# Performance work log

Hardware: AMD Instinct MI355X
Metric: run time of the kernel (lower is better)

## Reference

```python
import jax, jax.numpy as jnp
import numpy as np

BETA = 1.0  # config.beta
B, G, K, E2 = 1024, 512, 128, 128


def setup_inputs() -> dict:
    key = jax.random.key(0)
    k1, k2, k3, k4, k5 = jax.random.split(key, 5)
    s = 0.05
    return {
        "images": jax.random.normal(k1, (B, G), dtype=jnp.float32),
        "wimg": jax.random.normal(k2, (G, K), dtype=jnp.float32) * s,    # project.weight.T
        "wrec": jax.random.normal(k3, (K, E2), dtype=jnp.float32) * s,   # rec.weight.T
        "wrec2": jax.random.normal(k4, (K + 1, E2), dtype=jnp.float32) * s,  # rec2.weight.T
        "wimg2": jax.random.normal(k5, (G, K, K + 1), dtype=jnp.float32) * s,  # img2.weight.T.reshape(K+1,K,G).T
    }


def _soft_assign(x, codes):
    # x: [B, D], codes: [D, C] -> softmax over C of -beta * mean_D (x - codes)^2
    xh = -jnp.mean((x[:, :, None] - codes[None]) ** 2, axis=1) * BETA  # [B, C]
    return jax.nn.softmax(xh, axis=-1)


def reference(images, wimg, wrec, wrec2, wimg2):
    # ---- encode ----
    xp = _soft_assign(images, wimg)            # [B, K]
    lat = xp @ wrec                            # [B, E2]
    xp = _soft_assign(lat, wrec.T)             # [B, K] (codes are wrec.T: [E2, K])
    idx = jnp.argmax(xp, axis=-1)              # [B] hard component
    xwimg = jnp.transpose(wimg2[:, idx, :], (1, 0, 2))   # [B, G, K+1]
    base = wimg[:, idx].T[:, :, None]                     # [B, G, 1]
    xd = images[:, :, None] - base - xwimg                # [B, G, K+1]
    xh2 = -jnp.mean(xd ** 2, axis=1) * BETA               # [B, K+1]
    xp2 = jax.nn.softmax(xh2, axis=-1)
    lat2 = xp2 @ wrec2                                    # [B, E2]
    # ---- decode (ret='rec', n_step>=1) ----
    xp_d = _soft_assign(lat, wrec.T)           # [B, K]
    xp2_d = _soft_assign(lat2, wrec2.T)        # [B, K+1]
    wimgg = wimg[:, :, None] + wimg2           # [G, K, K+1]
    # tensordot(xp_d[:, :, None]*xp2_d[:, None, :], wimgg.permute(1,2,0), 2)
    xrec = jnp.einsum('bk,bj,gkj->bg', xp_d, xp2_d, wimgg)  # [B, G]
    # ---- loss ----
    loss = jnp.mean((xrec - images) ** 2, axis=-1)  # [B]
    return loss
```

## Files before the change

### kernel.cpp

```cpp
#include <hip/hip_runtime.h>

#define B_    1024
#define G_    512
#define K_    128
#define J_    129
#define JP_   132
#define E2_   128
#define KK_   16512
#define KK2_  16896
#define KKE2_ 17024
#define KKP_  17408
#define SPLITS 16
#define KCHUNK 1088
#define BK_   32
#define KSTEPS 34
#define GS_   8

using short8 = __attribute__((ext_vector_type(8))) short;
using f32x4  = __attribute__((ext_vector_type(4))) float;

__device__ __forceinline__ float bf2f(unsigned short h){
  return __uint_as_float(((unsigned int)h) << 16);
}
__device__ __forceinline__ unsigned short f2bf(float f){
  unsigned int u = __float_as_uint(f);
  u += 0x7fffu + ((u >> 16) & 1u);
  return (unsigned short)(u >> 16);
}

#define GLOAD16(gptr, ldst) __builtin_amdgcn_global_load_lds( \
    (const __attribute__((address_space(1))) unsigned int*)(gptr), \
    (__attribute__((address_space(3))) unsigned int*)(ldst), 16, 0, 0)

__device__ __forceinline__ float blockSum512(float v, float* red, int t){
  #pragma unroll
  for (int off = 32; off > 0; off >>= 1) v += __shfl_down(v, off);
  __syncthreads();
  if ((t & 63) == 0) red[t >> 6] = v;
  __syncthreads();
  float r = ((red[0] + red[1]) + (red[2] + red[3]))
          + ((red[4] + red[5]) + (red[6] + red[7]));
  __syncthreads();
  return r;
}

__device__ __forceinline__ void blockSoftmaxMS512(float x, bool act,
    float* redm, float* reds, int t, float& mo, float& so){
  float m = x, s = act ? 1.f : 0.f;
  #pragma unroll
  for (int off = 32; off > 0; off >>= 1){
    float om = __shfl_down(m, off);
    float os = __shfl_down(s, off);
    float nm = fmaxf(m, om);
    s = s*__expf(m - nm) + os*__expf(om - nm);
    m = nm;
  }
  __syncthreads();
  if ((t & 63) == 0){ redm[t >> 6] = m; reds[t >> 6] = s; }
  __syncthreads();
  float gm = redm[0], gsv = reds[0];
  #pragma unroll
  for (int w = 1; w < 8; w++){
    float om = redm[w], os = reds[w];
    float nm = fmaxf(gm, om);
    gsv = gsv*__expf(gm - nm) + os*__expf(om - nm);
    gm = nm;
  }
  mo = gm; so = gsv;
}

__device__ __forceinline__ int blockSoftmaxMSI512(float x, int idx, bool act,
    float* redm, float* reds, int* redi, int t, float& mo, float& so){
  float m = x, s = act ? 1.f : 0.f; int i = idx;
  #pragma unroll
  for (int off = 32; off > 0; off >>= 1){
    float om = __shfl_down(m, off);
    float os = __shfl_down(s, off);
    int   oi = __shfl_down(i, off);
    bool take = (om > m) || (om == m && oi < i);
    float nm = fmaxf(m, om);
    s = s*__expf(m - nm) + os*__expf(om - nm);
    i = take ? oi : i;
    m = nm;
  }
  __syncthreads();
  if ((t & 63) == 0){ redm[t >> 6] = m; reds[t >> 6] = s; redi[t >> 6] = i; }
  __syncthreads();
  float gm = redm[0], gsv = reds[0]; int gi = redi[0];
  #pragma unroll
  for (int w = 1; w < 8; w++){
    float om = redm[w], os = reds[w]; int oi = redi[w];
    bool take = (om > gm) || (om == gm && oi < gi);
    float nm = fmaxf(gm, om);
    gsv = gsv*__expf(gm - nm) + os*__expf(om - nm);
    gi = take ? oi : gi;
    gm = nm;
  }
  mo = gm; so = gsv;
  return gi;
}

__global__ __launch_bounds__(1024) void norms_kernel(
    const float* __restrict__ wimg, const float* __restrict__ wrec,
    const float* __restrict__ wrec2, float* __restrict__ c1norm,
    float* __restrict__ w3norm, float* __restrict__ w6norm,
    float* __restrict__ wrecT, float* __restrict__ wrec2T){
  int t = threadIdx.x;
  if (blockIdx.x == 0){
    __shared__ float red[8][128];
    int k = t & 127, sl = t >> 7;
    float s = 0.f;
    int g0 = sl * (G_/8);
    for (int g = g0; g < g0 + G_/8; g++){
      float v = wimg[g*K_ + k]; s += v*v;
    }
    red[sl][k] = s;
    __syncthreads();
    if (t < 128){
      float r = 0.f;
      #pragma unroll
      for (int i = 0; i < 8; i++) r += red[i][t];
      c1norm[t] = r;
    }
  } else if (blockIdx.x == 1){
    int wave = t >> 6, lane = t & 63;
    for (int k = wave; k < K_; k += 16){
      float v0 = wrec[k*E2_ + lane], v1 = wrec[k*E2_ + 64 + lane];
      float s = v0*v0 + v1*v1;
      #pragma unroll
      for (int off = 32; off > 0; off >>= 1) s += __shfl_down(s, off);
      if (lane == 0) w3norm[k] = s;
    }
  } else if (blockIdx.x == 2){
    int wave = t >> 6, lane = t & 63;
    for (int j = wave; j < J_; j += 16){
      float v0 = wrec2[j*E2_ + lane], v1 = wrec2[j*E2_ + 64 + lane];
      float s = v0*v0 + v1*v1;
      #pragma unroll
      for (int off = 32; off > 0; off >>= 1) s += __shfl_down(s, off);
      if (lane == 0) w6norm[j] = s;
    }
  } else if (blockIdx.x == 3){
    for (int n = t; n < K_*E2_; n += 1024){
      int k = n >> 7, e = n & 127;
      wrecT[e*K_ + k] = wrec[n];
    }
  } else {
    for (int n = t; n < J_*E2_; n += 1024){
      int j = n >> 7, e = n & 127;
      wrec2T[e*J_ + j] = wrec2[n];
    }
  }
}

__global__ __launch_bounds__(128) void tables_part_kernel(
    const float* __restrict__ wimg2, const float* __restrict__ wimg,
    float* __restrict__ sqp, float* __restrict__ crp,
    unsigned short* __restrict__ W2){
  int n  = blockIdx.x * 128 + threadIdx.x;
  int gs = blockIdx.y;
  int k = n / J_;
  int w2i = n + 3*k;
  float s0=0,s1=0,s2=0,s3=0, c0=0,c1=0,c2=0,c3=0;
  int gbase = gs * (G_/GS_);
  #pragma unroll 2
  for (int g = gbase; g < gbase + G_/GS_; g += 4){
    float w0 = wimg2[(size_t)(g  )*KK_ + n];
    float w1 = wimg2[(size_t)(g+1)*KK_ + n];
    float w2 = wimg2[(size_t)(g+2)*KK_ + n];
    float w3 = wimg2[(size_t)(g+3)*KK_ + n];
    W2[(size_t)(g  )*KKP_ + w2i] = f2bf(w0);
    W2[(size_t)(g+1)*KKP_ + w2i] = f2bf(w1);
    W2[(size_t)(g+2)*KKP_ + w2i] = f2bf(w2);
    W2[(size_t)(g+3)*KKP_ + w2i] = f2bf(w3);
    s0 += w0*w0; s1 += w1*w1; s2 += w2*w2; s3 += w3*w3;
    c0 += wimg[(g  )*K_ + k]*w0;
    c1 += wimg[(g+1)*K_ + k]*w1;
    c2 += wimg[(g+2)*K_ + k]*w2;
    c3 += wimg[(g+3)*K_ + k]*w3;
  }
  sqp[(size_t)gs*KK_ + n] = (s0+s1)+(s2+s3);
  crp[(size_t)gs*KK_ + n] = (c0+c1)+(c2+c3);
}
__global__ __launch_bounds__(128) void tables_reduce_kernel(
    const float* __restrict__ sqp, const float* __restrict__ crp,
    float* __restrict__ sq2, float* __restrict__ cross){
  int n = blockIdx.x * 128 + threadIdx.x;
  float s = 0.f, c = 0.f;
  #pragma unroll
  for (int gs = 0; gs < GS_; gs++){
    s += sqp[(size_t)gs*KK_ + n];
    c += crp[(size_t)gs*KK_ + n];
  }
  sq2[n] = s; cross[n] = c;
}

__global__ __launch_bounds__(128) void w2tail_kernel(
    const float* __restrict__ wimg, unsigned short* __restrict__ W2){
  int g = blockIdx.x, t = threadIdx.x;
  unsigned short* dst = W2 + (size_t)g * KKP_;
  dst[KK2_ + t]        = f2bf(wimg[g*K_ + t]);
  dst[KKE2_ + t]       = 0;
  dst[KKE2_ + 128 + t] = 0;
  dst[KKE2_ + 256 + t] = 0;
  dst[t*JP_ + 129] = 0;
  dst[t*JP_ + 130] = 0;
  dst[t*JP_ + 131] = 0;
}

__global__ __launch_bounds__(512, 8) void encdec_kernel(
    const float* __restrict__ img,  const float* __restrict__ wimg,
    const float* __restrict__ wrec, const float* __restrict__ wrec2,
    const float* __restrict__ wrecT, const float* __restrict__ wrec2T,
    const unsigned short* __restrict__ W2,
    const float* __restrict__ c1norm, const float* __restrict__ w3norm,
    const float* __restrict__ w6norm, const float* __restrict__ sq2,
    const float* __restrict__ cross, unsigned short* __restrict__ Rm){
  __shared__ __align__(16) float simg[G_];
  __shared__ float sp[K_];
  __shared__ float sqv[J_];
  __shared__ float slat[E2_];
  __shared__ float sd1[K_];
  __shared__ __align__(16) float sh16[16][128];
  __shared__ float sh4[4][K_];
  __shared__ float xtra[2];
  __shared__ float redm[8], reds[8];
  __shared__ int   redi[8];

  int t = threadIdx.x;
  int b = blockIdx.x;
  int tt = t & 127, q = t >> 7;
  int ll = t & 31, gq = t >> 5;

  simg[t] = img[b*G_ + t];
  __syncthreads();
  float a0 = simg[t];
  float imgnorm = blockSum512(a0*a0, redm, t);

  {
    float p0=0,p1=0,p2=0,p3=0;
    int g0 = gq * 32;
    #pragma unroll 4
    for (int g = g0; g < g0 + 32; g++){
      float4 wv = *(const float4*)(wimg + g*K_ + 4*ll);
      float sv = simg[g];
      p0 += sv*wv.x; p1 += sv*wv.y; p2 += sv*wv.z; p3 += sv*wv.w;
    }
    float4 st = {p0, p1, p2, p3};
    *(float4*)&sh16[gq][4*ll] = st;
  }
  __syncthreads();
  float xh1 = -3e38f, d1 = 0.f;
  if (t < 128){
    #pragma unroll
    for (int i = 0; i < 16; i++) d1 += sh16[i][t];
    sd1[t] = d1;
    xh1 = -(imgnorm - 2.f*d1 + c1norm[t]) * (1.f/512.f);
  }
  float m1, s1;
  blockSoftmaxMS512(xh1, t < 128, redm, reds, t, m1, s1);
  if (t < 128) sp[t] = __expf(xh1 - m1) / s1;
  __syncthreads();

  {
    float l0=0,l1=0;
    int k0 = q * 32;
    for (int k = k0; k < k0 + 32; k += 2){
      l0 += sp[k  ] * wrec[(k  )*E2_ + tt];
      l1 += sp[k+1] * wrec[(k+1)*E2_ + tt];
    }
    sh4[q][tt] = l0 + l1;
  }
  __syncthreads();
  float lat = (sh4[0][tt] + sh4[1][tt]) + (sh4[2][tt] + sh4[3][tt]);
  if (q == 0) slat[tt] = lat;
  float latnorm = blockSum512((q == 0) ? lat*lat : 0.f, redm, t);

  {
    float l0=0,l1=0;
    int e0 = q * 32;
    const float* rT = wrecT + tt;
    for (int e = e0; e < e0 + 32; e += 2){
      l0 += slat[e  ] * rT[(e  )*K_];
      l1 += slat[e+1] * rT[(e+1)*K_];
    }
    sh4[q][tt] = l0 + l1;
  }
  __syncthreads();
  float xh3 = -3e38f;
  if (t < 128){
    float d3 = (sh4[0][t] + sh4[1][t]) + (sh4[2][t] + sh4[3][t]);
    xh3 = -(latnorm - 2.f*d3 + w3norm[t]) * (1.f/128.f);
  }
  float m3, s3;
  int idxb = blockSoftmaxMSI512(xh3, tt, t < 128, redm, reds, redi, t, m3, s3);
  if (t < 128) sp[t] = __expf(xh3 - m3) / s3;
  float dsq = imgnorm - 2.f*sd1[idxb] + c1norm[idxb];

  {
    const unsigned short* Wb = W2 + (size_t)idxb * JP_ + 4*ll;
    float p0=0,p1=0,p2=0,p3=0;
    int g0 = gq * 32;
    #pragma unroll 4
    for (int g = g0; g < g0 + 32; g++){
      uint2 wv = *(const uint2*)(Wb + (size_t)g*KKP_);
      float sv = simg[g];
      p0 += sv * __uint_as_float(wv.x << 16);
      p1 += sv * __uint_as_float(wv.x & 0xffff0000u);
      p2 += sv * __uint_as_float(wv.y << 16);
      p3 += sv * __uint_as_float(wv.y & 0xffff0000u);
    }
    float4 st = {p0, p1, p2, p3};
    *(float4*)&sh16[gq][4*ll] = st;
  }
  if (t < 64){
    const unsigned short* Wb8 = W2 + (size_t)idxb * JP_ + 128;
    float s = 0.f;
    #pragma unroll
    for (int m = 0; m < 8; m++){
      int g = t + 64*m;
      s += simg[g] * bf2f(Wb8[(size_t)g * KKP_]);
    }
    #pragma unroll
    for (int off = 32; off > 0; off >>= 1) s += __shfl_down(s, off);
    if (t == 0) xtra[0] = s;
  }
  __syncthreads();
  float xh2 = -3e38f;
  if (t < J_){
    float di;
    if (t < 128){
      di = 0.f;
      #pragma unroll
      for (int i = 0; i < 16; i++) di += sh16[i][t];
    } else di = xtra[0];
    int nb = idxb*J_ + t;
    xh2 = -(dsq - 2.f*(di - cross[nb]) + sq2[nb]) * (1.f/512.f);
  }
  float m2, s2;
  blockSoftmaxMS512(xh2, t < J_, redm, reds, t, m2, s2);
  if (t < J_) sqv[t] = __expf(xh2 - m2) / s2;
  __syncthreads();

  {
    float lv = 0.f;
    int j0 = (q == 0) ? 0 : (q*32 + 1);
    int j1 = q*32 + 33;
    for (int j = j0; j < j1; j++)
      lv += sqv[j] * wrec2[j*E2_ + tt];
    sh4[q][tt] = lv;
  }
  __syncthreads();
  float lat2 = (sh4[0][tt] + sh4[1][tt]) + (sh4[2][tt] + sh4[3][tt]);
  if (q == 0) slat[tt] = lat2;
  float l2n = blockSum512((q == 0) ? lat2*lat2 : 0.f, redm, t);

  {
    float l0=0,l1=0;
    int e0 = q * 32;
    const float* rT = wrec2T + tt;
    for (int e = e0; e < e0 + 32; e += 2){
      l0 += slat[e  ] * rT[(e  )*J_];
      l1 += slat[e+1] * rT[(e+1)*J_];
    }
    sh4[q][tt] = l0 + l1;
  }
  if (t < 64){
    float s = slat[t]*wrec2T[t*J_ + 128] + slat[t+64]*wrec2T[(t+64)*J_ + 128];
    #pragma unroll
    for (int off = 32; off > 0; off >>= 1) s += __shfl_down(s, off);
    if (t == 0) xtra[1] = s;
  }
  __syncthreads();
  float xh6 = -3e38f;
  if (t < J_){
    float d6 = (t < 128) ? ((sh4[0][t] + sh4[1][t]) + (sh4[2][t] + sh4[3][t])) : xtra[1];
    xh6 = -(l2n - 2.f*d6 + w6norm[t]) * (1.f/128.f);
  }
  float m6, s6;
  blockSoftmaxMS512(xh6, t < J_, redm, reds, t, m6, s6);
  if (t < J_) sqv[t] = __expf(xh6 - m6) / s6;
  __syncthreads();

  unsigned int* Rrow32 = (unsigned int*)(Rm + (size_t)b * KKP_);
  int k = t / 66;
  int j2 = t - k*66;
  for (int kk2 = t; kk2 < KKP_/2; kk2 += 512){
    float v0 = 0.f, v1 = 0.f;
    if (kk2 < KK2_/2){
      int j = 2*j2;
      float pk = sp[k];
      v0 = (j   < J_) ? pk * sqv[j]   : 0.f;
      v1 = (j+1 < J_) ? pk * sqv[j+1] : 0.f;
    } else if (kk2 < KKE2_/2){
      int e = 2*(kk2 - KK2_/2);
      v0 = sp[e]; v1 = sp[e+1];
    }
    Rrow32[kk2] = (unsigned int)f2bf(v0) | ((unsigned int)f2bf(v1) << 16);
    j2 += 50;
    if (j2 >= 66){ j2 -= 66; k += 8; } else k += 7;
  }
}

__global__ __launch_bounds__(256) void gemm_kernel(
    const unsigned short* __restrict__ Rm, const unsigned short* __restrict__ W2,
    float* __restrict__ part){
  __shared__ __align__(16) unsigned int lds[8192];
  auto lds3 = (__attribute__((address_space(3))) unsigned int*)lds;
  int tid = threadIdx.x;
  int l = tid & 63;
  int wv = tid >> 6;
  int wr = (wv >> 1) * 64, wc = (wv & 1) * 64;
  int b0 = blockIdx.y * 128, g0 = blockIdx.x * 128;
  size_t kkbase = (size_t)blockIdx.z * KCHUNK;

  int srow = tid >> 2, scol = tid & 3;
  const unsigned short* ga  = Rm + (size_t)(b0 + srow)*KKP_ + kkbase + scol*8;
  const unsigned short* ga2 = ga + (size_t)64 * KKP_;
  const unsigned short* gb  = W2 + (size_t)(g0 + srow)*KKP_ + kkbase + scol*8;
  const unsigned short* gb2 = gb + (size_t)64 * KKP_;

  int lrow = l & 15, lko = (l >> 4) << 2;

  f32x4 zero4 = {0.f, 0.f, 0.f, 0.f};
  f32x4 acc[4][4];
  #pragma unroll
  for (int mi = 0; mi < 4; mi++)
    #pragma unroll
    for (int ni = 0; ni < 4; ni++) acc[mi][ni] = zero4;

  GLOAD16(ga,  lds3 + wv*256);
  GLOAD16(ga2, lds3 + 1024 + wv*256);
  GLOAD16(gb,  lds3 + 2048 + wv*256);
  GLOAD16(gb2, lds3 + 3072 + wv*256);
  ga += BK_; ga2 += BK_; gb += BK_; gb2 += BK_;

  int cur = 0;
  for (int s = 0; s < KSTEPS; s++){
    __syncthreads();
    if (s + 1 < KSTEPS){
      unsigned int nb = (cur ^ 1) * 4096;
      GLOAD16(ga,  lds3 + nb + wv*256);
      GLOAD16(ga2, lds3 + nb + 1024 + wv*256);
      GLOAD16(gb,  lds3 + nb + 2048 + wv*256);
      GLOAD16(gb2, lds3 + nb + 3072 + wv*256);
      ga += BK_; ga2 += BK_; gb += BK_; gb2 += BK_;
    }
    const unsigned int* lA = lds + cur*4096;
    const unsigned int* lB = lA + 2048;
    short8 af[4], bfv[4];
    #pragma unroll
    for (int mi = 0; mi < 4; mi++)
      af[mi] = *(const short8*)(lA + (wr + mi*16 + lrow)*16 + lko);
    #pragma unroll
    for (int ni = 0; ni < 4; ni++)
      bfv[ni] = *(const short8*)(lB + (wc + ni*16 + lrow)*16 + lko);
    #pragma unroll
    for (int mi = 0; mi < 4; mi++)
      #pragma unroll
      for (int ni = 0; ni < 4; ni++)
        acc[mi][ni] = __builtin_amdgcn_mfma_f32_16x16x32_bf16(af[mi], bfv[ni], acc[mi][ni], 0, 0, 0);
    cur ^= 1;
  }

  float* P = part + ((size_t)blockIdx.z * B_ + b0) * G_ + g0;
  int rh = (l >> 4) << 2, cl = l & 15;
  #pragma unroll
  for (int mi = 0; mi < 4; mi++)
    #pragma unroll
    for (int ni = 0; ni < 4; ni++)
      #pragma unroll
      for (int r = 0; r < 4; r++){
        int row = wr + mi*16 + rh + r;
        int col = wc + ni*16 + cl;
        P[(size_t)row*G_ + col] = acc[mi][ni][r];
      }
}

__global__ __launch_bounds__(128) void loss_kernel(
    const float* __restrict__ img, const float* __restrict__ part,
    float* __restrict__ out){
  __shared__ float redf[2];
  int t = threadIdx.x, b = blockIdx.x;
  float acc = 0.f;
  for (int g = t; g < G_; g += 128){
    float x = 0.f;
    #pragma unroll
    for (int z = 0; z < SPLITS; z++)
      x += part[((size_t)z*B_ + b)*G_ + g];
    float d = x - img[b*G_ + g];
    acc += d*d;
  }
  #pragma unroll
  for (int off = 32; off > 0; off >>= 1) acc += __shfl_down(acc, off);
  __syncthreads();
  if ((t & 63) == 0) redf[t >> 6] = acc;
  __syncthreads();
  if (t == 0) out[b] = (redf[0] + redf[1]) * (1.f/512.f);
}

extern "C" void kernel_launch(void* const* d_in, const int* in_sizes, int n_in,
                              void* d_out, int out_size, void* d_ws, size_t ws_size,
                              hipStream_t stream){
  (void)in_sizes; (void)n_in; (void)out_size; (void)ws_size;
  const float* img   = (const float*)d_in[0];
  const float* wimg  = (const float*)d_in[1];
  const float* wrec  = (const float*)d_in[2];
  const float* wrec2 = (const float*)d_in[3];
  const float* wimg2 = (const float*)d_in[4];
  float* out = (float*)d_out;

  char* ws = (char*)d_ws;
  size_t off = 0;
  auto alloc = [&](size_t bytes) -> void* {
    void* p = ws + off;
    off += (bytes + 255) & ~(size_t)255;
    return p;
  };
  unsigned short* W2   = (unsigned short*)alloc((size_t)G_ * KKP_ * 2);
  unsigned short* Rm   = (unsigned short*)alloc((size_t)B_ * KKP_ * 2);
  float* part   = (float*)alloc((size_t)SPLITS * B_ * G_ * 4);
  float* sqp    = (float*)alloc((size_t)GS_ * KK_ * 4);
  float* crp    = (float*)alloc((size_t)GS_ * KK_ * 4);
  float* sq2    = (float*)alloc((size_t)KK_ * 4);
  float* cross  = (float*)alloc((size_t)KK_ * 4);
  float* c1norm = (float*)alloc(K_ * 4);
  float* w3norm = (float*)alloc(K_ * 4);
  float* w6norm = (float*)alloc(J_ * 4);
  float* wrecT  = (float*)alloc((size_t)K_ * E2_ * 4);
  float* wrec2T = (float*)alloc((size_t)J_ * E2_ * 4);

  norms_kernel<<<dim3(5), dim3(1024), 0, stream>>>(wimg, wrec, wrec2, c1norm, w3norm, w6norm, wrecT, wrec2T);
  tables_part_kernel<<<dim3(129, GS_), dim3(128), 0, stream>>>(wimg2, wimg, sqp, crp, W2);
  tables_reduce_kernel<<<dim3(129), dim3(128), 0, stream>>>(sqp, crp, sq2, cross);
  w2tail_kernel<<<dim3(512), dim3(128), 0, stream>>>(wimg, W2);
  encdec_kernel<<<dim3(1024), dim3(512), 0, stream>>>(img, wimg, wrec, wrec2, wrecT, wrec2T, W2,
      c1norm, w3norm, w6norm, sq2, cross, Rm);
  gemm_kernel<<<dim3(4, 8, SPLITS), dim3(256), 0, stream>>>(Rm, W2, part);
  loss_kernel<<<dim3(1024), dim3(128), 0, stream>>>(img, part, out);
}
```

Measured before the change: 122.9 us.

## Process two batch rows per encdec block to share weight loads and barriers

The encode/decode kernel now handles two images per block: each weight element loaded from global memory (wimg, wrec, wrecT, wrec2, wrec2T) is reused for both rows, and the block reductions and softmaxes are paired so each barrier serves two rows. The grid halves to 512 blocks and the occupancy hint drops from 8 to 4 blocks per CU to give room for the extra registers. The cost is fewer blocks on the GPU, which leaves less parallelism to hide latency, plus doubled LDS use per block. The gather of W2 rows through idx stays per-row.

```diff
diff --git a/kernel.cpp b/kernel.cpp
--- a/kernel.cpp
+++ b/kernel.cpp
@@ -32,72 +32,96 @@
     (const __attribute__((address_space(1))) unsigned int*)(gptr), \
     (__attribute__((address_space(3))) unsigned int*)(ldst), 16, 0, 0)
 
-__device__ __forceinline__ float blockSum512(float v, float* red, int t){
-  #pragma unroll
-  for (int off = 32; off > 0; off >>= 1) v += __shfl_down(v, off);
-  __syncthreads();
-  if ((t & 63) == 0) red[t >> 6] = v;
-  __syncthreads();
-  float r = ((red[0] + red[1]) + (red[2] + red[3]))
-          + ((red[4] + red[5]) + (red[6] + red[7]));
-  __syncthreads();
-  return r;
-}
-
-__device__ __forceinline__ void blockSoftmaxMS512(float x, bool act,
-    float* redm, float* reds, int t, float& mo, float& so){
-  float m = x, s = act ? 1.f : 0.f;
+__device__ __forceinline__ void blockSum2(float v0, float v1, float* red, int t,
+                                          float& r0, float& r1){
   #pragma unroll
   for (int off = 32; off > 0; off >>= 1){
-    float om = __shfl_down(m, off);
-    float os = __shfl_down(s, off);
-    float nm = fmaxf(m, om);
-    s = s*__expf(m - nm) + os*__expf(om - nm);
-    m = nm;
-  }
-  __syncthreads();
-  if ((t & 63) == 0){ redm[t >> 6] = m; reds[t >> 6] = s; }
-  __syncthreads();
-  float gm = redm[0], gsv = reds[0];
+    v0 += __shfl_down(v0, off);
+    v1 += __shfl_down(v1, off);
+  }
+  __syncthreads();
+  if ((t & 63) == 0){ red[t >> 6] = v0; red[8 + (t >> 6)] = v1; }
+  __syncthreads();
+  r0 = ((red[0] + red[1]) + (red[2] + red[3])) + ((red[4] + red[5]) + (red[6] + red[7]));
+  r1 = ((red[8] + red[9]) + (red[10] + red[11])) + ((red[12] + red[13]) + (red[14] + red[15]));
+  __syncthreads();
+}
+
+__device__ __forceinline__ void blockSoftmaxMS2(float x0, float x1, bool act,
+    float* redm, float* reds, int t,
+    float& m0o, float& s0o, float& m1o, float& s1o){
+  float m0 = x0, s0 = act ? 1.f : 0.f;
+  float m1 = x1, s1 = act ? 1.f : 0.f;
+  #pragma unroll
+  for (int off = 32; off > 0; off >>= 1){
+    float om0 = __shfl_down(m0, off), os0 = __shfl_down(s0, off);
+    float om1 = __shfl_down(m1, off), os1 = __shfl_down(s1, off);
+    float nm0 = fmaxf(m0, om0);
+    s0 = s0*__expf(m0 - nm0) + os0*__expf(om0 - nm0); m0 = nm0;
+    float nm1 = fmaxf(m1, om1);
+    s1 = s1*__expf(m1 - nm1) + os1*__expf(om1 - nm1); m1 = nm1;
+  }
+  __syncthreads();
+  if ((t & 63) == 0){
+    redm[t >> 6] = m0; reds[t >> 6] = s0;
+    redm[8 + (t >> 6)] = m1; reds[8 + (t >> 6)] = s1;
+  }
+  __syncthreads();
+  float gm0 = redm[0], gs0 = reds[0], gm1 = redm[8], gs1 = reds[8];
   #pragma unroll
   for (int w = 1; w < 8; w++){
-    float om = redm[w], os = reds[w];
-    float nm = fmaxf(gm, om);
-    gsv = gsv*__expf(gm - nm) + os*__expf(om - nm);
-    gm = nm;
-  }
-  mo = gm; so = gsv;
-}
-
-__device__ __forceinline__ int blockSoftmaxMSI512(float x, int idx, bool act,
-    float* redm, float* reds, int* redi, int t, float& mo, float& so){
-  float m = x, s = act ? 1.f : 0.f; int i = idx;
+    float om0 = redm[w], os0 = reds[w];
+    float nm0 = fmaxf(gm0, om0);
+    gs0 = gs0*__expf(gm0 - nm0) + os0*__expf(om0 - nm0); gm0 = nm0;
+    float om1 = redm[8 + w], os1 = reds[8 + w];
+    float nm1 = fmaxf(gm1, om1);
+    gs1 = gs1*__expf(gm1 - nm1) + os1*__expf(om1 - nm1); gm1 = nm1;
+  }
+  m0o = gm0; s0o = gs0; m1o = gm1; s1o = gs1;
+}
+
+__device__ __forceinline__ void blockSoftmaxMSI2(float x0, float x1, int idx, bool act,
+    float* redm, float* reds, int* redi, int t,
+    float& m0o, float& s0o, int& i0o, float& m1o, float& s1o, int& i1o){
+  float m0 = x0, s0 = act ? 1.f : 0.f; int i0 = idx;
+  float m1 = x1, s1 = act ? 1.f : 0.f; int i1 = idx;
   #pragma unroll
   for (int off = 32; off > 0; off >>= 1){
-    float om = __shfl_down(m, off);
-    float os = __shfl_down(s, off);
-    int   oi = __shfl_down(i, off);
-    bool take = (om > m) || (om == m && oi < i);
-    float nm = fmaxf(m, om);
-    s = s*__expf(m - nm) + os*__expf(om - nm);
-    i = take ? oi : i;
-    m = nm;
-  }
-  __syncthreads();
-  if ((t & 63) == 0){ redm[t >> 6] = m; reds[t >> 6] = s; redi[t >> 6] = i; }
-  __syncthreads();
-  float gm = redm[0], gsv = reds[0]; int gi = redi[0];
+    float om0 = __shfl_down(m0, off), os0 = __shfl_down(s0, off);
+    int   oi0 = __shfl_down(i0, off);
+    float om1 = __shfl_down(m1, off), os1 = __shfl_down(s1, off);
+    int   oi1 = __shfl_down(i1, off);
+    bool tk0 = (om0 > m0) || (om0 == m0 && oi0 < i0);
+    float nm0 = fmaxf(m0, om0);
+    s0 = s0*__expf(m0 - nm0) + os0*__expf(om0 - nm0);
+    i0 = tk0 ? oi0 : i0; m0 = nm0;
+    bool tk1 = (om1 > m1) || (om1 == m1 && oi1 < i1);
+    float nm1 = fmaxf(m1, om1);
+    s1 = s1*__expf(m1 - nm1) + os1*__expf(om1 - nm1);
+    i1 = tk1 ? oi1 : i1; m1 = nm1;
+  }
+  __syncthreads();
+  if ((t & 63) == 0){
+    redm[t >> 6] = m0; reds[t >> 6] = s0; redi[t >> 6] = i0;
+    redm[8 + (t >> 6)] = m1; reds[8 + (t >> 6)] = s1; redi[8 + (t >> 6)] = i1;
+  }
+  __syncthreads();
+  float gm0 = redm[0], gs0 = reds[0]; int gi0 = redi[0];
+  float gm1 = redm[8], gs1 = reds[8]; int gi1 = redi[8];
   #pragma unroll
   for (int w = 1; w < 8; w++){
-    float om = redm[w], os = reds[w]; int oi = redi[w];
-    bool take = (om > gm) || (om == gm && oi < gi);
-    float nm = fmaxf(gm, om);
-    gsv = gsv*__expf(gm - nm) + os*__expf(om - nm);
-    gi = take ? oi : gi;
-    gm = nm;
-  }
-  mo = gm; so = gsv;
-  return gi;
+    { float om = redm[w], os = reds[w]; int oi = redi[w];
+      bool tk = (om > gm0) || (om == gm0 && oi < gi0);
+      float nm = fmaxf(gm0, om);
+      gs0 = gs0*__expf(gm0 - nm) + os*__expf(om - nm);
+      gi0 = tk ? oi : gi0; gm0 = nm; }
+    { float om = redm[8 + w], os = reds[8 + w]; int oi = redi[8 + w];
+      bool tk = (om > gm1) || (om == gm1 && oi < gi1);
+      float nm = fmaxf(gm1, om);
+      gs1 = gs1*__expf(gm1 - nm) + os*__expf(om - nm);
+      gi1 = tk ? oi : gi1; gm1 = nm; }
+  }
+  m0o = gm0; s0o = gs0; i0o = gi0; m1o = gm1; s1o = gs1; i1o = gi1;
 }
 
 __global__ __launch_bounds__(1024) void norms_kernel(
@@ -208,7 +232,7 @@
   dst[t*JP_ + 131] = 0;
 }
 
-__global__ __launch_bounds__(512, 8) void encdec_kernel(
+__global__ __launch_bounds__(512, 4) void encdec_kernel(
     const float* __restrict__ img,  const float* __restrict__ wimg,
     const float* __restrict__ wrec, const float* __restrict__ wrec2,
     const float* __restrict__ wrecT, const float* __restrict__ wrec2T,
@@ -216,187 +240,251 @@
     const float* __restrict__ c1norm, const float* __restrict__ w3norm,
     const float* __restrict__ w6norm, const float* __restrict__ sq2,
     const float* __restrict__ cross, unsigned short* __restrict__ Rm){
-  __shared__ __align__(16) float simg[G_];
-  __shared__ float sp[K_];
-  __shared__ float sqv[J_];
-  __shared__ float slat[E2_];
-  __shared__ float sd1[K_];
-  __shared__ __align__(16) float sh16[16][128];
-  __shared__ float sh4[4][K_];
-  __shared__ float xtra[2];
-  __shared__ float redm[8], reds[8];
-  __shared__ int   redi[8];
+  __shared__ __align__(16) float simg[2][G_];
+  __shared__ float sp[2][K_];
+  __shared__ float sqv[2][JP_];
+  __shared__ float slat[2][E2_];
+  __shared__ float sd1[2][K_];
+  __shared__ __align__(16) float sh16a[16][128];
+  __shared__ __align__(16) float sh16b[16][128];
+  __shared__ float sh4a[4][K_], sh4b[4][K_];
+  __shared__ float xtra[4];
+  __shared__ float redm[16], reds[16];
+  __shared__ int   redi[16];
 
   int t = threadIdx.x;
-  int b = blockIdx.x;
+  int b0 = blockIdx.x * 2, b1 = b0 + 1;
   int tt = t & 127, q = t >> 7;
   int ll = t & 31, gq = t >> 5;
-
-  simg[t] = img[b*G_ + t];
-  __syncthreads();
-  float a0 = simg[t];
-  float imgnorm = blockSum512(a0*a0, redm, t);
+  int wvid = t >> 6, lane = t & 63;
+
+  simg[0][t] = img[b0*G_ + t];
+  simg[1][t] = img[b1*G_ + t];
+  __syncthreads();
+  float a0 = simg[0][t], a1 = simg[1][t];
+  float in0, in1;
+  blockSum2(a0*a0, a1*a1, redm, t, in0, in1);
 
   {
-    float p0=0,p1=0,p2=0,p3=0;
+    float p00=0,p01=0,p02=0,p03=0, p10=0,p11=0,p12=0,p13=0;
     int g0 = gq * 32;
     #pragma unroll 4
     for (int g = g0; g < g0 + 32; g++){
       float4 wv = *(const float4*)(wimg + g*K_ + 4*ll);
-      float sv = simg[g];
-      p0 += sv*wv.x; p1 += sv*wv.y; p2 += sv*wv.z; p3 += sv*wv.w;
-    }
-    float4 st = {p0, p1, p2, p3};
-    *(float4*)&sh16[gq][4*ll] = st;
-  }
-  __syncthreads();
-  float xh1 = -3e38f, d1 = 0.f;
+      float sv0 = simg[0][g], sv1 = simg[1][g];
+      p00 += sv0*wv.x; p01 += sv0*wv.y; p02 += sv0*wv.z; p03 += sv0*wv.w;
+      p10 += sv1*wv.x; p11 += sv1*wv.y; p12 += sv1*wv.z; p13 += sv1*wv.w;
+    }
+    float4 st0 = {p00,p01,p02,p03};
+    float4 st1 = {p10,p11,p12,p13};
+    *(float4*)&sh16a[gq][4*ll] = st0;
+    *(float4*)&sh16b[gq][4*ll] = st1;
+  }
+  __syncthreads();
+  float xh10 = -3e38f, xh11 = -3e38f;
   if (t < 128){
-    #pragma unroll
-    for (int i = 0; i < 16; i++) d1 += sh16[i][t];
-    sd1[t] = d1;
-    xh1 = -(imgnorm - 2.f*d1 + c1norm[t]) * (1.f/512.f);
-  }
-  float m1, s1;
-  blockSoftmaxMS512(xh1, t < 128, redm, reds, t, m1, s1);
-  if (t < 128) sp[t] = __expf(xh1 - m1) / s1;
+    float d0 = 0.f, d1 = 0.f;
+    #pragma unroll
+    for (int i = 0; i < 16; i++){ d0 += sh16a[i][t]; d1 += sh16b[i][t]; }
+    sd1[0][t] = d0; sd1[1][t] = d1;
+    xh10 = -(in0 - 2.f*d0 + c1norm[t]) * (1.f/512.f);
+    xh11 = -(in1 - 2.f*d1 + c1norm[t]) * (1.f/512.f);
+  }
+  float m10, s10, m11, s11;
+  blockSoftmaxMS2(xh10, xh11, t < 128, redm, reds, t, m10, s10, m11, s11);
+  if (t < 128){
+    sp[0][t] = __expf(xh10 - m10) / s10;
+    sp[1][t] = __expf(xh11 - m11) / s11;
+  }
   __syncthreads();
 
   {
-    float l0=0,l1=0;
+    float l00=0,l01=0, l10=0,l11=0;
     int k0 = q * 32;
     for (int k = k0; k < k0 + 32; k += 2){
-      l0 += sp[k  ] * wrec[(k  )*E2_ + tt];
-      l1 += sp[k+1] * wrec[(k+1)*E2_ + tt];
-    }
-    sh4[q][tt] = l0 + l1;
-  }
-  __syncthreads();
-  float lat = (sh4[0][tt] + sh4[1][tt]) + (sh4[2][tt] + sh4[3][tt]);
-  if (q == 0) slat[tt] = lat;
-  float latnorm = blockSum512((q == 0) ? lat*lat : 0.f, redm, t);
+      float w0 = wrec[(k  )*E2_ + tt];
+      float w1 = wrec[(k+1)*E2_ + tt];
+      l00 += sp[0][k]*w0; l01 += sp[0][k+1]*w1;
+      l10 += sp[1][k]*w0; l11 += sp[1][k+1]*w1;
+    }
+    sh4a[q][tt] = l00 + l01;
+    sh4b[q][tt] = l10 + l11;
+  }
+  __syncthreads();
+  float lat0 = (sh4a[0][tt] + sh4a[1][tt]) + (sh4a[2][tt] + sh4a[3][tt]);
+  float lat1 = (sh4b[0][tt] + sh4b[1][tt]) + (sh4b[2][tt] + sh4b[3][tt]);
+  if (q == 0){ slat[0][tt] = lat0; slat[1][tt] = lat1; }
+  float ln0, ln1;
+  blockSum2((q == 0) ? lat0*lat0 : 0.f, (q == 0) ? lat1*lat1 : 0.f, redm, t, ln0, ln1);
 
   {
-    float l0=0,l1=0;
+    float l00=0,l01=0, l10=0,l11=0;
     int e0 = q * 32;
     const float* rT = wrecT + tt;
     for (int e = e0; e < e0 + 32; e += 2){
-      l0 += slat[e  ] * rT[(e  )*K_];
-      l1 += slat[e+1] * rT[(e+1)*K_];
-    }
-    sh4[q][tt] = l0 + l1;
-  }
-  __syncthreads();
-  float xh3 = -3e38f;
+      float w0 = rT[(e  )*K_];
+      float w1 = rT[(e+1)*K_];
+      l00 += slat[0][e]*w0; l01 += slat[0][e+1]*w1;
+      l10 += slat[1][e]*w0; l11 += slat[1][e+1]*w1;
+    }
+    sh4a[q][tt] = l00 + l01;
+    sh4b[q][tt] = l10 + l11;
+  }
+  __syncthreads();
+  float xh30 = -3e38f, xh31 = -3e38f;
   if (t < 128){
-    float d3 = (sh4[0][t] + sh4[1][t]) + (sh4[2][t] + sh4[3][t]);
-    xh3 = -(latnorm - 2.f*d3 + w3norm[t]) * (1.f/128.f);
-  }
-  float m3, s3;
-  int idxb = blockSoftmaxMSI512(xh3, tt, t < 128, redm, reds, redi, t, m3, s3);
-  if (t < 128) sp[t] = __expf(xh3 - m3) / s3;
-  float dsq = imgnorm - 2.f*sd1[idxb] + c1norm[idxb];
+    float d30 = (sh4a[0][t] + sh4a[1][t]) + (sh4a[2][t] + sh4a[3][t]);
+    float d31 = (sh4b[0][t] + sh4b[1][t]) + (sh4b[2][t] + sh4b[3][t]);
+    xh30 = -(ln0 - 2.f*d30 + w3norm[t]) * (1.f/128.f);
+    xh31 = -(ln1 - 2.f*d31 + w3norm[t]) * (1.f/128.f);
+  }
+  float m30, s30, m31, s31; int idx0, idx1;
+  blockSoftmaxMSI2(xh30, xh31, tt, t < 128, redm, reds, redi, t,
+                   m30, s30, idx0, m31, s31, idx1);
+  if (t < 128){
+    sp[0][t] = __expf(xh30 - m30) / s30;
+    sp[1][t] = __expf(xh31 - m31) / s31;
+  }
+  float dsq0 = in0 - 2.f*sd1[0][idx0] + c1norm[idx0];
+  float dsq1 = in1 - 2.f*sd1[1][idx1] + c1norm[idx1];
 
   {
-    const unsigned short* Wb = W2 + (size_t)idxb * JP_ + 4*ll;
-    float p0=0,p1=0,p2=0,p3=0;
+    const unsigned short* Wb0 = W2 + (size_t)idx0 * JP_ + 4*ll;
+    const unsigned short* Wb1 = W2 + (size_t)idx1 * JP_ + 4*ll;
+    float p00=0,p01=0,p02=0,p03=0, p10=0,p11=0,p12=0,p13=0;
     int g0 = gq * 32;
-    #pragma unroll 4
+    #pragma unroll 2
     for (int g = g0; g < g0 + 32; g++){
-      uint2 wv = *(const uint2*)(Wb + (size_t)g*KKP_);
-      float sv = simg[g];
-      p0 += sv * __uint_as_float(wv.x << 16);
-      p1 += sv * __uint_as_float(wv.x & 0xffff0000u);
-      p2 += sv * __uint_as_float(wv.y << 16);
-      p3 += sv * __uint_as_float(wv.y & 0xffff0000u);
-    }
-    float4 st = {p0, p1, p2, p3};
-    *(float4*)&sh16[gq][4*ll] = st;
-  }
-  if (t < 64){
-    const unsigned short* Wb8 = W2 + (size_t)idxb * JP_ + 128;
+      uint2 w0 = *(const uint2*)(Wb0 + (size_t)g*KKP_);
+      uint2 w1 = *(const uint2*)(Wb1 + (size_t)g*KKP_);
+      float sv0 = simg[0][g], sv1 = simg[1][g];
+      p00 += sv0 * __uint_as_float(w0.x << 16);
+      p01 += sv0 * __uint_as_float(w0.x & 0xffff0000u);
+      p02 += sv0 * __uint_as_float(w0.y << 16);
+      p03 += sv0 * __uint_as_float(w0.y & 0xffff0000u);
+      p10 += sv1 * __uint_as_float(w1.x << 16);
+      p11 += sv1 * __uint_as_float(w1.x & 0xffff0000u);
+      p12 += sv1 * __uint_as_float(w1.y << 16);
+      p13 += sv1 * __uint_as_float(w1.y & 0xffff0000u);
+    }
+    float4 st0 = {p00,p01,p02,p03};
+    float4 st1 = {p10,p11,p12,p13};
+    *(float4*)&sh16a[gq][4*ll] = st0;
+    *(float4*)&sh16b[gq][4*ll] = st1;
+  }
+  if (wvid < 2){
+    int ib = wvid ? idx1 : idx0;
+    const float* si = simg[wvid];
+    const unsigned short* Wb8 = W2 + (size_t)ib * JP_ + 128;
     float s = 0.f;
     #pragma unroll
     for (int m = 0; m < 8; m++){
-      int g = t + 64*m;
-      s += simg[g] * bf2f(Wb8[(size_t)g * KKP_]);
+      int g = lane + 64*m;
+      s += si[g] * bf2f(Wb8[(size_t)g * KKP_]);
     }
     #pragma unroll
     for (int off = 32; off > 0; off >>= 1) s += __shfl_down(s, off);
-    if (t == 0) xtra[0] = s;
-  }
-  __syncthreads();
-  float xh2 = -3e38f;
+    if (lane == 0) xtra[wvid] = s;
+  }
+  __syncthreads();
+  float xh20 = -3e38f, xh21 = -3e38f;
   if (t < J_){
-    float di;
+    float di0, di1;
     if (t < 128){
-      di = 0.f;
+      di0 = 0.f; di1 = 0.f;
       #pragma unroll
-      for (int i = 0; i < 16; i++) di += sh16[i][t];
-    } else di = xtra[0];
-    int nb = idxb*J_ + t;
-    xh2 = -(dsq - 2.f*(di - cross[nb]) + sq2[nb]) * (1.f/512.f);
-  }
-  float m2, s2;
-  blockSoftmaxMS512(xh2, t < J_, redm, reds, t, m2, s2);
-  if (t < J_) sqv[t] = __expf(xh2 - m2) / s2;
+      for (int i = 0; i < 16; i++){ di0 += sh16a[i][t]; di1 += sh16b[i][t]; }
+    } else { di0 = xtra[0]; di1 = xtra[1]; }
+    int nb0 = idx0*J_ + t, nb1 = idx1*J_ + t;
+    xh20 = -(dsq0 - 2.f*(di0 - cross[nb0]) + sq2[nb0]) * (1.f/512.f);
+    xh21 = -(dsq1 - 2.f*(di1 - cross[nb1]) + sq2[nb1]) * (1.f/512.f);
+  }
+  float m20, s20, m21, s21;
+  blockSoftmaxMS2(xh20, xh21, t < J_, redm, reds, t, m20, s20, m21, s21);
+  if (t < J_){
+    sqv[0][t] = __expf(xh20 - m20) / s20;
+    sqv[1][t] = __expf(xh21 - m21) / s21;
+  }
   __syncthreads();
 
   {
-    float lv = 0.f;
+    float lv0 = 0.f, lv1 = 0.f;
     int j0 = (q == 0) ? 0 : (q*32 + 1);
     int j1 = q*32 + 33;
-    for (int j = j0; j < j1; j++)
-      lv += sqv[j] * wrec2[j*E2_ + tt];
-    sh4[q][tt] = lv;
-  }
-  __syncthreads();
-  float lat2 = (sh4[0][tt] + sh4[1][tt]) + (sh4[2][tt] + sh4[3][tt]);
-  if (q == 0) slat[tt] = lat2;
-  float l2n = blockSum512((q == 0) ? lat2*lat2 : 0.f, redm, t);
+    for (int j = j0; j < j1; j++){
+      float w = wrec2[j*E2_ + tt];
+      lv0 += sqv[0][j]*w; lv1 += sqv[1][j]*w;
+    }
+    sh4a[q][tt] = lv0;
+    sh4b[q][tt] = lv1;
+  }
+  __syncthreads();
+  float l20 = (sh4a[0][tt] + sh4a[1][tt]) + (sh4a[2][tt] + sh4a[3][tt]);
+  float l21 = (sh4b[0][tt] + sh4b[1][tt]) + (sh4b[2][tt] + sh4b[3][tt]);
+  if (q == 0){ slat[0][tt] = l20; slat[1][tt] = l21; }
+  float n20, n21;
+  blockSum2((q == 0) ? l20*l20 : 0.f, (q == 0) ? l21*l21 : 0.f, redm, t, n20, n21);
 
   {
-    float l0=0,l1=0;
+    float l00=0,l01=0, l10=0,l11=0;
     int e0 = q * 32;
     const float* rT = wrec2T + tt;
     for (int e = e0; e < e0 + 32; e += 2){
-      l0 += slat[e  ] * rT[(e  )*J_];
-      l1 += slat[e+1] * rT[(e+1)*J_];
-    }
-    sh4[q][tt] = l0 + l1;
-  }
-  if (t < 64){
-    float s = slat[t]*wrec2T[t*J_ + 128] + slat[t+64]*wrec2T[(t+64)*J_ + 128];
+      float w0 = rT[(e  )*J_];
+      float w1 = rT[(e+1)*J_];
+      l00 += slat[0][e]*w0; l01 += slat[0][e+1]*w1;
+      l10 += slat[1][e]*w0; l11 += slat[1][e+1]*w1;
+    }
+    sh4a[q][tt] = l00 + l01;
+    sh4b[q][tt] = l10 + l11;
+  }
+  if (wvid < 2){
+    const float* sl = slat[wvid];
+    float s = sl[lane]*wrec2T[lane*J_ + 128] + sl[lane+64]*wrec2T[(lane+64)*J_ + 128];
     #pragma unroll
     for (int off = 32; off > 0; off >>= 1) s += __shfl_down(s, off);
-    if (t == 0) xtra[1] = s;
-  }
-  __syncthreads();
-  float xh6 = -3e38f;
+    if (lane == 0) xtra[2 + wvid] = s;
+  }
+  __syncthreads();
+  float xh60 = -3e38f, xh61 = -3e38f;
   if (t < J_){
-    float d6 = (t < 128) ? ((sh4[0][t] + sh4[1][t]) + (sh4[2][t] + sh4[3][t])) : xtra[1];
-    xh6 = -(l2n - 2.f*d6 + w6norm[t]) * (1.f/128.f);
-  }
-  float m6, s6;
-  blockSoftmaxMS512(xh6, t < J_, redm, reds, t, m6, s6);
-  if (t < J_) sqv[t] = __expf(xh6 - m6) / s6;
-  __syncthreads();
-
-  unsigned int* Rrow32 = (unsigned int*)(Rm + (size_t)b * KKP_);
+    float d60, d61;
+    if (t < 128){
+      d60 = (sh4a[0][t] + sh4a[1][t]) + (sh4a[2][t] + sh4a[3][t]);
+      d61 = (sh4b[0][t] + sh4b[1][t]) + (sh4b[2][t] + sh4b[3][t]);
+    } else { d60 = xtra[2]; d61 = xtra[3]; }
+    xh60 = -(n20 - 2.f*d60 + w6norm[t]) * (1.f/128.f);
+    xh61 = -(n21 - 2.f*d61 + w6norm[t]) * (1.f/128.f);
+  }
+  float m60, s60, m61, s61;
+  blockSoftmaxMS2(xh60, xh61, t < J_, redm, reds, t, m60, s60, m61, s61);
+  if (t < J_){
+    sqv[0][t] = __expf(xh60 - m60) / s60;
+    sqv[1][t] = __expf(xh61 - m61) / s61;
+  }
+  __syncthreads();
+
+  unsigned int* R0 = (unsigned int*)(Rm + (size_t)b0 * KKP_);
+  unsigned int* R1 = (unsigned int*)(Rm + (size_t)b1 * KKP_);
   int k = t / 66;
   int j2 = t - k*66;
   for (int kk2 = t; kk2 < KKP_/2; kk2 += 512){
-    float v0 = 0.f, v1 = 0.f;
+    float v00 = 0.f, v01 = 0.f, v10 = 0.f, v11 = 0.f;
     if (kk2 < KK2_/2){
       int j = 2*j2;
-      float pk = sp[k];
-      v0 = (j   < J_) ? pk * sqv[j]   : 0.f;
-      v1 = (j+1 < J_) ? pk * sqv[j+1] : 0.f;
+      float pk0 = sp[0][k], pk1 = sp[1][k];
+      bool jo0 = (j < J_), jo1 = (j+1 < J_);
+      v00 = jo0 ? pk0 * sqv[0][j]   : 0.f;
+      v01 = jo1 ? pk0 * sqv[0][j+1] : 0.f;
+      v10 = jo0 ? pk1 * sqv[1][j]   : 0.f;
+      v11 = jo1 ? pk1 * sqv[1][j+1] : 0.f;
     } else if (kk2 < KKE2_/2){
       int e = 2*(kk2 - KK2_/2);
-      v0 = sp[e]; v1 = sp[e+1];
-    }
-    Rrow32[kk2] = (unsigned int)f2bf(v0) | ((unsigned int)f2bf(v1) << 16);
+      v00 = sp[0][e]; v01 = sp[0][e+1];
+      v10 = sp[1][e]; v11 = sp[1][e+1];
+    }
+    R0[kk2] = (unsigned int)f2bf(v00) | ((unsigned int)f2bf(v01) << 16);
+    R1[kk2] = (unsigned int)f2bf(v10) | ((unsigned int)f2bf(v11) << 16);
     j2 += 50;
     if (j2 >= 66){ j2 -= 66; k += 8; } else k += 7;
   }
@@ -534,7 +622,7 @@
   tables_part_kernel<<<dim3(129, GS_), dim3(128), 0, stream>>>(wimg2, wimg, sqp, crp, W2);
   tables_reduce_kernel<<<dim3(129), dim3(128), 0, stream>>>(sqp, crp, sq2, cross);
   w2tail_kernel<<<dim3(512), dim3(128), 0, stream>>>(wimg, W2);
-  encdec_kernel<<<dim3(1024), dim3(512), 0, stream>>>(img, wimg, wrec, wrec2, wrecT, wrec2T, W2,
+  encdec_kernel<<<dim3(512), dim3(512), 0, stream>>>(img, wimg, wrec, wrec2, wrecT, wrec2T, W2,
       c1norm, w3norm, w6norm, sq2, cross, Rm);
   gemm_kernel<<<dim3(4, 8, SPLITS), dim3(256), 0, stream>>>(Rm, W2, part);
   loss_kernel<<<dim3(1024), dim3(128), 0, stream>>>(img, part, out);
```

New measurement: 116.4 us. 5.3% less time.

## Widen GEMM K-step with swizzled LDS, store bf16 partials, vectorize loss reduction

Applied to the files above, without the earlier changes.

Doubles the GEMM K tile to 64 (half as many barriers) and applies an XOR swizzle to the LDS layout so fragment reads avoid bank conflicts. The split-K partial sums are now stored as bf16 rather than fp32, which halves the partial-buffer write and read traffic. The loss kernel reads four partials per thread with vector loads. GS_ is also raised to 16, which changes the table-partial split. Rounding the partials to bf16 loses some precision in the reconstruction before the loss is taken.

```diff
diff --git a/kernel.cpp b/kernel.cpp
--- a/kernel.cpp
+++ b/kernel.cpp
@@ -12,9 +12,9 @@
 #define KKP_  17408
 #define SPLITS 16
 #define KCHUNK 1088
-#define BK_   32
-#define KSTEPS 34
-#define GS_   8
+#define BK_   64
+#define KSTEPS 17
+#define GS_   16
 
 using short8 = __attribute__((ext_vector_type(8))) short;
 using f32x4  = __attribute__((ext_vector_type(4))) float;
@@ -404,8 +404,8 @@
 
 __global__ __launch_bounds__(256) void gemm_kernel(
     const unsigned short* __restrict__ Rm, const unsigned short* __restrict__ W2,
-    float* __restrict__ part){
-  __shared__ __align__(16) unsigned int lds[8192];
+    unsigned short* __restrict__ part){
+  __shared__ __align__(16) unsigned int lds[16384];
   auto lds3 = (__attribute__((address_space(3))) unsigned int*)lds;
   int tid = threadIdx.x;
   int l = tid & 63;
@@ -414,13 +414,12 @@
   int b0 = blockIdx.y * 128, g0 = blockIdx.x * 128;
   size_t kkbase = (size_t)blockIdx.z * KCHUNK;
 
-  int srow = tid >> 2, scol = tid & 3;
-  const unsigned short* ga  = Rm + (size_t)(b0 + srow)*KKP_ + kkbase + scol*8;
-  const unsigned short* ga2 = ga + (size_t)64 * KKP_;
-  const unsigned short* gb  = W2 + (size_t)(g0 + srow)*KKP_ + kkbase + scol*8;
-  const unsigned short* gb2 = gb + (size_t)64 * KKP_;
-
-  int lrow = l & 15, lko = (l >> 4) << 2;
+  int srow = tid >> 3;
+  int cswz = (tid & 7) ^ (srow & 7);
+  const unsigned short* ga = Rm + (size_t)(b0 + srow)*KKP_ + kkbase + cswz*8;
+  const unsigned short* gb = W2 + (size_t)(g0 + srow)*KKP_ + kkbase + cswz*8;
+
+  int lrow = l & 15, lh = l >> 4, p7 = l & 7;
 
   f32x4 zero4 = {0.f, 0.f, 0.f, 0.f};
   f32x4 acc[4][4];
@@ -429,41 +428,43 @@
     #pragma unroll
     for (int ni = 0; ni < 4; ni++) acc[mi][ni] = zero4;
 
-  GLOAD16(ga,  lds3 + wv*256);
-  GLOAD16(ga2, lds3 + 1024 + wv*256);
-  GLOAD16(gb,  lds3 + 2048 + wv*256);
-  GLOAD16(gb2, lds3 + 3072 + wv*256);
-  ga += BK_; ga2 += BK_; gb += BK_; gb2 += BK_;
-
+  auto STAGE = [&](int bb){
+    unsigned int base = bb * 8192;
+    #pragma unroll
+    for (int c = 0; c < 4; c++){
+      GLOAD16(ga + (size_t)c*32*KKP_, lds3 + base + c*1024 + wv*256);
+      GLOAD16(gb + (size_t)c*32*KKP_, lds3 + base + 4096 + c*1024 + wv*256);
+    }
+    ga += BK_; gb += BK_;
+  };
+
+  STAGE(0);
   int cur = 0;
   for (int s = 0; s < KSTEPS; s++){
     __syncthreads();
-    if (s + 1 < KSTEPS){
-      unsigned int nb = (cur ^ 1) * 4096;
-      GLOAD16(ga,  lds3 + nb + wv*256);
-      GLOAD16(ga2, lds3 + nb + 1024 + wv*256);
-      GLOAD16(gb,  lds3 + nb + 2048 + wv*256);
-      GLOAD16(gb2, lds3 + nb + 3072 + wv*256);
-      ga += BK_; ga2 += BK_; gb += BK_; gb2 += BK_;
-    }
-    const unsigned int* lA = lds + cur*4096;
-    const unsigned int* lB = lA + 2048;
-    short8 af[4], bfv[4];
-    #pragma unroll
-    for (int mi = 0; mi < 4; mi++)
-      af[mi] = *(const short8*)(lA + (wr + mi*16 + lrow)*16 + lko);
-    #pragma unroll
-    for (int ni = 0; ni < 4; ni++)
-      bfv[ni] = *(const short8*)(lB + (wc + ni*16 + lrow)*16 + lko);
-    #pragma unroll
-    for (int mi = 0; mi < 4; mi++)
+    if (s + 1 < KSTEPS) STAGE(cur ^ 1);
+    const unsigned int* lA = lds + cur*8192;
+    const unsigned int* lB = lA + 4096;
+    #pragma unroll
+    for (int s2 = 0; s2 < 2; s2++){
+      int slot = ((s2 << 2) + lh) ^ p7;
+      short8 af[4], bfv[4];
+      #pragma unroll
+      for (int mi = 0; mi < 4; mi++)
+        af[mi] = *(const short8*)(lA + (wr + mi*16 + lrow)*32 + slot*4);
       #pragma unroll
       for (int ni = 0; ni < 4; ni++)
-        acc[mi][ni] = __builtin_amdgcn_mfma_f32_16x16x32_bf16(af[mi], bfv[ni], acc[mi][ni], 0, 0, 0);
+        bfv[ni] = *(const short8*)(lB + (wc + ni*16 + lrow)*32 + slot*4);
+      #pragma unroll
+      for (int mi = 0; mi < 4; mi++)
+        #pragma unroll
+        for (int ni = 0; ni < 4; ni++)
+          acc[mi][ni] = __builtin_amdgcn_mfma_f32_16x16x32_bf16(af[mi], bfv[ni], acc[mi][ni], 0, 0, 0);
+    }
     cur ^= 1;
   }
 
-  float* P = part + ((size_t)blockIdx.z * B_ + b0) * G_ + g0;
+  unsigned short* P = part + ((size_t)blockIdx.z * B_ + b0) * G_ + g0;
   int rh = (l >> 4) << 2, cl = l & 15;
   #pragma unroll
   for (int mi = 0; mi < 4; mi++)
@@ -473,24 +474,28 @@
       for (int r = 0; r < 4; r++){
         int row = wr + mi*16 + rh + r;
         int col = wc + ni*16 + cl;
-        P[(size_t)row*G_ + col] = acc[mi][ni][r];
+        P[(size_t)row*G_ + col] = f2bf(acc[mi][ni][r]);
       }
 }
 
 __global__ __launch_bounds__(128) void loss_kernel(
-    const float* __restrict__ img, const float* __restrict__ part,
+    const float* __restrict__ img, const unsigned short* __restrict__ part,
     float* __restrict__ out){
   __shared__ float redf[2];
   int t = threadIdx.x, b = blockIdx.x;
-  float acc = 0.f;
-  for (int g = t; g < G_; g += 128){
-    float x = 0.f;
-    #pragma unroll
-    for (int z = 0; z < SPLITS; z++)
-      x += part[((size_t)z*B_ + b)*G_ + g];
-    float d = x - img[b*G_ + g];
-    acc += d*d;
-  }
+  float x0 = 0.f, x1 = 0.f, x2 = 0.f, x3 = 0.f;
+  #pragma unroll
+  for (int z = 0; z < SPLITS; z++){
+    const unsigned short* pr = part + ((size_t)z*B_ + b)*G_ + 4*t;
+    uint2 v = *(const uint2*)pr;
+    x0 += __uint_as_float(v.x << 16);
+    x1 += __uint_as_float(v.x & 0xffff0000u);
+    x2 += __uint_as_float(v.y << 16);
+    x3 += __uint_as_float(v.y & 0xffff0000u);
+  }
+  float4 iv = *(const float4*)(img + (size_t)b*G_ + 4*t);
+  float d0 = x0 - iv.x, d1 = x1 - iv.y, d2 = x2 - iv.z, d3 = x3 - iv.w;
+  float acc = (d0*d0 + d1*d1) + (d2*d2 + d3*d3);
   #pragma unroll
   for (int off = 32; off > 0; off >>= 1) acc += __shfl_down(acc, off);
   __syncthreads();
@@ -519,7 +524,7 @@
   };
   unsigned short* W2   = (unsigned short*)alloc((size_t)G_ * KKP_ * 2);
   unsigned short* Rm   = (unsigned short*)alloc((size_t)B_ * KKP_ * 2);
-  float* part   = (float*)alloc((size_t)SPLITS * B_ * G_ * 4);
+  unsigned short* part = (unsigned short*)alloc((size_t)SPLITS * B_ * G_ * 2);
   float* sqp    = (float*)alloc((size_t)GS_ * KK_ * 4);
   float* crp    = (float*)alloc((size_t)GS_ * KK_ * 4);
   float* sq2    = (float*)alloc((size_t)KK_ * 4);
```

Measured after the change: 118.9 us. -3.3%, faster.
